# Kernel optimization log

Hardware: AMD Instinct MI355X
Metric: run time of the kernel (lower is better)

The kernel has to match this reference:

```python
import jax, jax.numpy as jnp
import numpy as np

N = 1_000_000   # active voxels
CIN = 32
COUT = 64
K = 9           # 3x3 kernel offsets (rulebook size)
EPS = 1e-5


def setup_inputs() -> dict:
    key = jax.random.key(0)
    ks = jax.random.split(key, 6)
    x = jax.random.normal(ks[0], (N, CIN), dtype=jnp.float32)
    # rulebook: neighbor index per (voxel, kernel offset); stride=1 so same coord set
    nbr = jax.random.randint(ks[1], (N, K), 0, N, dtype=jnp.int32)
    W1 = jax.random.normal(ks[2], (K, CIN, COUT), dtype=jnp.float32) * (1.0 / np.sqrt(K * CIN))
    W2 = jax.random.normal(ks[3], (K, COUT, COUT), dtype=jnp.float32) * (1.0 / np.sqrt(K * COUT))
    Wd = jax.random.normal(ks[4], (CIN, COUT), dtype=jnp.float32) * (1.0 / np.sqrt(CIN))
    g1 = jnp.ones((COUT,), jnp.float32); b1 = jnp.zeros((COUT,), jnp.float32)
    g2 = jnp.ones((COUT,), jnp.float32); b2 = jnp.zeros((COUT,), jnp.float32)
    gd = jnp.ones((COUT,), jnp.float32); bd = jnp.zeros((COUT,), jnp.float32)
    return {"x": x, "W1": W1, "g1": g1, "b1": b1, "W2": W2, "g2": g2, "b2": b2,
            "Wd": Wd, "gd": gd, "bd": bd, "nbr": nbr}


def _sparse_conv(x, nbr, W):
    # gather-GEMM-scatter; loop over the fixed K=9 kernel offsets to avoid
    # materializing the full [N, K, Cin] gathered tensor
    out = jnp.zeros((x.shape[0], W.shape[-1]), dtype=x.dtype)
    for k in range(W.shape[0]):
        out = out + jnp.take(x, nbr[:, k], axis=0) @ W[k]
    return out


def _bn(x, gamma, beta):
    # BatchNorm1d over the voxel dimension (training-mode batch statistics)
    mu = jnp.mean(x, axis=0)
    var = jnp.var(x, axis=0)
    return gamma * (x - mu) * jax.lax.rsqrt(var + EPS) + beta


def reference(x, W1, g1, b1, W2, g2, b2, Wd, gd, bd, nbr):
    # downsample branch (1x1 conv -> BN, no relu) since in_ch != out_ch
    identity = _bn(x @ Wd, gd, bd)
    # conv1: SparseConv3x3 -> BN -> ReLU
    out = jax.nn.relu(_bn(_sparse_conv(x, nbr, W1), g1, b1))
    # conv2: SparseConv3x3 -> BN (no relu)
    out = _bn(_sparse_conv(out, nbr, W2), g2, b2)
    # residual add + final ReLU
    return jax.nn.relu(out + identity)
```

## Files before the change

kernel.cpp:

```cpp
#include <hip/hip_runtime.h>
#include <hip/hip_bf16.h>

#define NV 1000000
#define CI 32
#define CO 64
#define KK 9
#define NG (NV / 16)
#define EPSV 1e-5f

typedef __bf16 bf16x8 __attribute__((ext_vector_type(8)));
typedef float  f32x4  __attribute__((ext_vector_type(4)));

__device__ __forceinline__ f32x4 mfma16(bf16x8 a, bf16x8 b, f32x4 c) {
    return __builtin_amdgcn_mfma_f32_16x16x32_bf16(a, b, c, 0, 0, 0);
}

__device__ __forceinline__ float xredseg(float v) {
    v += __shfl_xor(v, 16, 64);
    v += __shfl_xor(v, 32, 64);
    return v;
}

__global__ void k_prep_w(const float* __restrict__ W1, const float* __restrict__ W2,
                         const float* __restrict__ Wd,
                         __bf16* __restrict__ W1T, __bf16* __restrict__ W2T,
                         __bf16* __restrict__ WdT) {
    int i = blockIdx.x * blockDim.x + threadIdx.x;
    const int n1 = KK * CO * CI;
    const int n2 = KK * CO * CO;
    const int nd = CO * CI;
    if (i < n1) {
        int k = i / (CO * CI), r = i % (CO * CI), co = r / CI, ci = r % CI;
        W1T[i] = (__bf16)W1[(k * CI + ci) * CO + co];
    } else if (i < n1 + n2) {
        int j = i - n1;
        int k = j / (CO * CO), r = j % (CO * CO), co = r / CO, ci = r % CO;
        W2T[j] = (__bf16)W2[(k * CO + ci) * CO + co];
    } else if (i < n1 + n2 + nd) {
        int j = i - n1 - n2;
        int co = j / CI, ci = j % CI;
        WdT[j] = (__bf16)Wd[ci * CO + co];
    }
}

__global__ void k_prep_x(const float* __restrict__ x, __bf16* __restrict__ xb) {
    int i = blockIdx.x * blockDim.x + threadIdx.x;
    const float4* px = (const float4*)x + 2 * (size_t)i;
    float4 u = px[0], v = px[1];
    bf16x8 o;
    o[0] = (__bf16)u.x; o[1] = (__bf16)u.y; o[2] = (__bf16)u.z; o[3] = (__bf16)u.w;
    o[4] = (__bf16)v.x; o[5] = (__bf16)v.y; o[6] = (__bf16)v.z; o[7] = (__bf16)v.w;
    *((bf16x8*)xb + i) = o;
}

__global__ __launch_bounds__(256, 2) void k_conv1(
    const __bf16* __restrict__ xb, const int* __restrict__ nbr,
    const __bf16* __restrict__ W1T, const __bf16* __restrict__ WdT,
    __bf16* __restrict__ y1b, float* __restrict__ stats) {
    __shared__ __align__(16) char w1smem[KK * CO * CI * 2];

    const int lane = threadIdx.x & 63;
    const int w    = threadIdx.x >> 6;
    const int r    = lane & 15;
    const int seg  = lane >> 4;

#pragma unroll
    for (int j = 0; j < 9; j++) {
        const __bf16* srcp = W1T + (size_t)(j * 256 + threadIdx.x) * 8;
        __builtin_amdgcn_global_load_lds(
            (const __attribute__((address_space(1))) void*)srcp,
            (__attribute__((address_space(3))) void*)(w1smem + j * 4096 + w * 1024),
            16, 0, 0);
    }
    __syncthreads();

    bf16x8 wd[4];
#pragma unroll
    for (int t = 0; t < 4; t++)
        wd[t] = *(const bf16x8*)(WdT + (size_t)(t * 16 + r) * CI + seg * 8);

    float ps1[4] = {0.f,0.f,0.f,0.f}, pq1[4] = {0.f,0.f,0.f,0.f};
    float psd[4] = {0.f,0.f,0.f,0.f}, pqd[4] = {0.f,0.f,0.f,0.f};

    const int slot   = blockIdx.x * 4 + w;
    const int stride = gridDim.x * 4;
    const f32x4 z = {0.f, 0.f, 0.f, 0.f};

    auto loadIdx = [&](int (&idx)[KK], int tile) {
        const int* nb = nbr + (size_t)(tile * 16 + r) * KK;
#pragma unroll
        for (int k = 0; k < KK; k++) idx[k] = nb[k];
    };
    auto gather9 = [&](bf16x8 (&g)[KK], const int (&idx)[KK]) {
#pragma unroll
        for (int k = 0; k < KK; k++)
            g[k] = *(const bf16x8*)(xb + (size_t)idx[k] * CI + seg * 8);
    };
    auto loadAd = [&](int tile) {
        return *(const bf16x8*)(xb + (size_t)(tile * 16 + r) * CI + seg * 8);
    };
    auto compute = [&](int tile, const bf16x8 (&g)[KK], bf16x8 ad) {
        int w1off = 0;
        asm volatile("" : "+v"(w1off));
        const __bf16* wb = (const __bf16*)w1smem + w1off;

        f32x4 acc[4]  = {z, z, z, z};
        f32x4 accd[4] = {z, z, z, z};
#pragma unroll
        for (int t = 0; t < 4; t++) accd[t] = mfma16(ad, wd[t], accd[t]);
#pragma unroll
        for (int k = 0; k < KK; k++) {
#pragma unroll
            for (int t = 0; t < 4; t++) {
                bf16x8 b = *(const bf16x8*)(wb + k * 2048 + t * 512 + r * 32 + seg * 8);
                acc[t] = mfma16(g[k], b, acc[t]);
            }
        }

        const int vb = tile * 16;
#pragma unroll
        for (int t = 0; t < 4; t++) {
#pragma unroll
            for (int rr = 0; rr < 4; rr++) {
                float val = acc[t][rr];
                int row = vb + seg * 4 + rr;
                __builtin_nontemporal_store((__bf16)val, &y1b[(size_t)row * CO + t * 16 + r]);
                ps1[t] += val; pq1[t] += val * val;
                float dv = accd[t][rr];
                psd[t] += dv; pqd[t] += dv * dv;
            }
        }
    };

    int idx0[KK], idx1[KK];
    bf16x8 g0[KK], g1[KK];
    bf16x8 ad0, ad1;

    int it = slot;
    loadIdx(idx0, it);
    gather9(g0, idx0); ad0 = loadAd(it);
    int itn = it + stride;
    bool have = (itn < NG);
    if (have) loadIdx(idx1, itn);

    while (true) {
        if (have) {
            gather9(g1, idx1); ad1 = loadAd(itn);
            int it2 = itn + stride;
            if (it2 < NG) loadIdx(idx0, it2);
        }
        compute(it, g0, ad0);
        if (!have) break;
        it = itn; itn = it + stride; have = (itn < NG);

        if (have) {
            gather9(g0, idx0); ad0 = loadAd(itn);
            int it2 = itn + stride;
            if (it2 < NG) loadIdx(idx1, it2);
        }
        compute(it, g1, ad1);
        if (!have) break;
        it = itn; itn = it + stride; have = (itn < NG);
    }

#pragma unroll
    for (int t = 0; t < 4; t++) {
        ps1[t] = xredseg(ps1[t]); pq1[t] = xredseg(pq1[t]);
        psd[t] = xredseg(psd[t]); pqd[t] = xredseg(pqd[t]);
    }
    if (lane < 16) {
#pragma unroll
        for (int t = 0; t < 4; t++) {
            atomicAdd(&stats[0 * 64 + t * 16 + lane], ps1[t]);
            atomicAdd(&stats[1 * 64 + t * 16 + lane], pq1[t]);
            atomicAdd(&stats[2 * 64 + t * 16 + lane], psd[t]);
            atomicAdd(&stats[3 * 64 + t * 16 + lane], pqd[t]);
        }
    }
}

#define TILE_B (16 * KK * 128)

__global__ __launch_bounds__(128, 2) void k_conv2(
    const __bf16* __restrict__ h1b, const int* __restrict__ nbr,
    const __bf16* __restrict__ W2T, const float* __restrict__ g1,
    const float* __restrict__ b1,
    float* __restrict__ y2, float* __restrict__ stats) {
    __shared__ __align__(16) char smem[2][TILE_B];

    const int lane = threadIdx.x & 63;
    const int w    = threadIdx.x >> 6;
    const int r    = lane & 15;
    const int seg  = lane >> 4;
    const int p    = lane & 7;

    bf16x8 w2[KK][2][2];
#pragma unroll
    for (int k = 0; k < KK; k++)
#pragma unroll
        for (int t2 = 0; t2 < 2; t2++)
#pragma unroll
            for (int s = 0; s < 2; s++) {
                int co = w * 32 + t2 * 16 + r;
                int ci = s * 32 + seg * 8;
                w2[k][t2][s] = *(const bf16x8*)(W2T + ((size_t)(k * CO + co)) * CO + ci);
            }

    float scP[8], shP[8];
#pragma unroll
    for (int j = 0; j < 8; j++) {
        int c0 = p * 8 + j;
        float mu  = stats[c0] * (1.0f / NV);
        float var = stats[64 + c0] * (1.0f / NV) - mu * mu;
        float s   = g1[c0] * rsqrtf(var + EPSV);
        scP[j] = s; shP[j] = b1[c0] - mu * s;
    }

    int ri[9], dstoff[9];
#pragma unroll
    for (int s = 0; s < 9; s++) {
        int c = w * 576 + s * 64 + lane;
        int rIdx = c >> 3;
        int i = (rIdx * 57) >> 9;
        ri[s] = rIdx;
        dstoff[s] = rIdx * 128 + ((p ^ (i & 7)) * 16);
    }

    auto loadIdx = [&](int (&ix)[9], int tile) {
        const int* nb = nbr + (size_t)tile * (16 * KK);
#pragma unroll
        for (int s = 0; s < 9; s++) ix[s] = nb[ri[s]];
    };
    auto loadDat = [&](f32x4 (&d)[9], const int (&ix)[9]) {
#pragma unroll
        for (int s = 0; s < 9; s++)
            d[s] = *(const f32x4*)(h1b + (size_t)ix[s] * CO + p * 8);
    };
    auto xform = [&](char* tb, const f32x4 (&d)[9]) {
#pragma unroll
        for (int s = 0; s < 9; s++) {
            union { f32x4 f; bf16x8 b; } u; u.f = d[s];
            bf16x8 o;
#pragma unroll
            for (int j = 0; j < 8; j++)
                o[j] = (__bf16)fmaxf((float)u.b[j] * scP[j] + shP[j], 0.f);
            *(bf16x8*)(tb + dstoff[s]) = o;
        }
    };

    float ps[2] = {0.f, 0.f}, pq[2] = {0.f, 0.f};
    const f32x4 z = {0.f, 0.f, 0.f, 0.f};
    const int sw = r & 7;
    const int G = gridDim.x;

    int idxN[9]; f32x4 dat[9];
    int it = blockIdx.x;
    loadIdx(idxN, it);
    loadDat(dat, idxN);
    { int t1 = it + G;     loadIdx(idxN, t1 < NG ? t1 : NG - 1); }
    xform(smem[0], dat);
    loadDat(dat, idxN);
    { int t2 = it + 2 * G; loadIdx(idxN, t2 < NG ? t2 : NG - 1); }
    __syncthreads();
    int cur = 0;

    for (; it < NG; it += G) {
        const __bf16* base = (const __bf16*)smem[cur];
        f32x4 acc[2] = {z, z};
#pragma unroll
        for (int k = 0; k < KK; k++) {
            const __bf16* rp = base + (size_t)(r * KK + k) * 64;
            bf16x8 a0 = *(const bf16x8*)(rp + ((seg ^ sw) * 8));
            bf16x8 a1 = *(const bf16x8*)(rp + (((4 + seg) ^ sw) * 8));
            acc[0] = mfma16(a0, w2[k][0][0], acc[0]);
            acc[0] = mfma16(a1, w2[k][0][1], acc[0]);
            acc[1] = mfma16(a0, w2[k][1][0], acc[1]);
            acc[1] = mfma16(a1, w2[k][1][1], acc[1]);
        }

        const int vb = it * 16;
#pragma unroll
        for (int t2 = 0; t2 < 2; t2++) {
#pragma unroll
            for (int rr = 0; rr < 4; rr++) {
                float val = acc[t2][rr];
                int row = vb + seg * 4 + rr;
                int c = w * 32 + t2 * 16 + r;
                __builtin_nontemporal_store(val, &y2[(size_t)row * CO + c]);
                ps[t2] += val; pq[t2] += val * val;
            }
        }

        int nx = it + G;
        if (nx < NG) {
            xform(smem[cur ^ 1], dat);
            loadDat(dat, idxN);
            { int t3 = it + 3 * G; loadIdx(idxN, t3 < NG ? t3 : NG - 1); }
            __syncthreads();
            cur ^= 1;
        }
    }

#pragma unroll
    for (int t2 = 0; t2 < 2; t2++) { ps[t2] = xredseg(ps[t2]); pq[t2] = xredseg(pq[t2]); }
    if (lane < 16) {
#pragma unroll
        for (int t2 = 0; t2 < 2; t2++) {
            atomicAdd(&stats[4 * 64 + w * 32 + t2 * 16 + lane], ps[t2]);
            atomicAdd(&stats[5 * 64 + w * 32 + t2 * 16 + lane], pq[t2]);
        }
    }
}

__global__ __launch_bounds__(256, 2) void k_final(
    const __bf16* __restrict__ xb, const __bf16* __restrict__ WdT,
    float* __restrict__ out, const float* __restrict__ stats,
    const float* __restrict__ g2, const float* __restrict__ b2,
    const float* __restrict__ gd, const float* __restrict__ bd) {
    __shared__ float s2[CO], sh2[CO], sdv[CO], shd[CO];
    int t = threadIdx.x;
    if (t < CO) {
        float mu2  = stats[4 * 64 + t] * (1.0f / NV);
        float var2 = stats[5 * 64 + t] * (1.0f / NV) - mu2 * mu2;
        float s = g2[t] * rsqrtf(var2 + EPSV);
        s2[t] = s; sh2[t] = b2[t] - mu2 * s;
        float mud  = stats[2 * 64 + t] * (1.0f / NV);
        float vard = stats[3 * 64 + t] * (1.0f / NV) - mud * mud;
        float sd = gd[t] * rsqrtf(vard + EPSV);
        sdv[t] = sd; shd[t] = bd[t] - mud * sd;
    }
    __syncthreads();

    const int lane = threadIdx.x & 63;
    const int w    = threadIdx.x >> 6;
    const int r    = lane & 15;
    const int seg  = lane >> 4;

    bf16x8 wd[4];
#pragma unroll
    for (int t4 = 0; t4 < 4; t4++)
        wd[t4] = *(const bf16x8*)(WdT + (size_t)(t4 * 16 + r) * CI + seg * 8);

    const int slot = blockIdx.x * 4 + w;
    const int nslots = gridDim.x * 4;
    const f32x4 z = {0.f, 0.f, 0.f, 0.f};

    for (int gid = slot; gid < NG; gid += nslots) {
        const int vb = gid * 16;
        const int v  = vb + r;
        bf16x8 ad = *(const bf16x8*)(xb + (size_t)v * CI + seg * 8);
        f32x4 accd[4] = {z, z, z, z};
#pragma unroll
        for (int t4 = 0; t4 < 4; t4++) accd[t4] = mfma16(ad, wd[t4], accd[t4]);
#pragma unroll
        for (int t4 = 0; t4 < 4; t4++) {
#pragma unroll
            for (int rr = 0; rr < 4; rr++) {
                int row = vb + seg * 4 + rr;
                int c = t4 * 16 + r;
                size_t o = (size_t)row * CO + c;
                float y2v = out[o];
                float res = s2[c] * y2v + sh2[c] + sdv[c] * accd[t4][rr] + shd[c];
                out[o] = fmaxf(res, 0.f);
            }
        }
    }
}

extern "C" void kernel_launch(void* const* d_in, const int* in_sizes, int n_in,
                              void* d_out, int out_size, void* d_ws, size_t ws_size,
                              hipStream_t stream) {
    const float* x  = (const float*)d_in[0];
    const float* W1 = (const float*)d_in[1];
    const float* g1 = (const float*)d_in[2];
    const float* b1 = (const float*)d_in[3];
    const float* W2 = (const float*)d_in[4];
    const float* g2 = (const float*)d_in[5];
    const float* b2 = (const float*)d_in[6];
    const float* Wd = (const float*)d_in[7];
    const float* gd = (const float*)d_in[8];
    const float* bd = (const float*)d_in[9];
    const int*  nbr = (const int*)d_in[10];

    char* ws = (char*)d_ws;
    __bf16* xb  = (__bf16*)ws;
    __bf16* y1b = (__bf16*)(ws + 64000000);
    __bf16* W1T = (__bf16*)(ws + 192000000);
    __bf16* W2T = W1T + KK * CO * CI;
    __bf16* WdT = W2T + KK * CO * CO;
    float* stats = (float*)(ws + 192000000 + 2 * (KK*CO*CI + KK*CO*CO + CO*CI));

    hipMemsetAsync(stats, 0, 6 * 64 * sizeof(float), stream);

    int nprep = KK*CO*CI + KK*CO*CO + CO*CI;
    k_prep_w<<<(nprep + 255) / 256, 256, 0, stream>>>(W1, W2, Wd, W1T, W2T, WdT);
    k_prep_x<<<(NV * CI / 8) / 256, 256, 0, stream>>>(x, xb);
    k_conv1<<<1024, 256, 0, stream>>>(xb, nbr, W1T, WdT, y1b, stats);
    k_conv2<<<1024, 128, 0, stream>>>(y1b, nbr, W2T, g1, b1, (float*)d_out, stats);
    k_final<<<1024, 256, 0, stream>>>(xb, WdT, (float*)d_out, stats, g2, b2, gd, bd);
}
```

Baseline: 617.1 us.

## Swap MFMA operands for row-contiguous vector stores and store conv2 output as bf16

The MFMA operands are swapped so each lane holds four consecutive output channels of one voxel. Each lane can then write them with a single vector store instead of four scattered scalar stores in conv1, conv2 and the final kernel. conv2 now writes its intermediate as bf16 into a new workspace region when the workspace is large enough, which halves that round-trip traffic. The per-channel stats reduction is reworked for the new layout, and the conv1 grid shrinks to 768 blocks. The bf16 intermediate adds rounding error to the conv2 output before the final BN.

```diff
diff --git a/kernel.cpp b/kernel.cpp
--- a/kernel.cpp
+++ b/kernel.cpp
@@ -9,6 +9,7 @@
 #define EPSV 1e-5f
 
 typedef __bf16 bf16x8 __attribute__((ext_vector_type(8)));
+typedef __bf16 bf16x4 __attribute__((ext_vector_type(4)));
 typedef float  f32x4  __attribute__((ext_vector_type(4)));
 
 __device__ __forceinline__ f32x4 mfma16(bf16x8 a, bf16x8 b, f32x4 c) {
@@ -18,6 +19,13 @@
 __device__ __forceinline__ float xredseg(float v) {
     v += __shfl_xor(v, 16, 64);
     v += __shfl_xor(v, 32, 64);
+    return v;
+}
+__device__ __forceinline__ float xred16(float v) {
+    v += __shfl_xor(v, 1, 64);
+    v += __shfl_xor(v, 2, 64);
+    v += __shfl_xor(v, 4, 64);
+    v += __shfl_xor(v, 8, 64);
     return v;
 }
 
@@ -79,7 +87,11 @@
     for (int t = 0; t < 4; t++)
         wd[t] = *(const bf16x8*)(WdT + (size_t)(t * 16 + r) * CI + seg * 8);
 
-    float ps1[4] = {0.f,0.f,0.f,0.f}, pq1[4] = {0.f,0.f,0.f,0.f};
+    float ps1[4][4], pq1[4][4];
+#pragma unroll
+    for (int t = 0; t < 4; t++)
+#pragma unroll
+        for (int rr = 0; rr < 4; rr++) { ps1[t][rr] = 0.f; pq1[t][rr] = 0.f; }
     float psd[4] = {0.f,0.f,0.f,0.f}, pqd[4] = {0.f,0.f,0.f,0.f};
 
     const int slot   = blockIdx.x * 4 + w;
@@ -113,22 +125,23 @@
 #pragma unroll
             for (int t = 0; t < 4; t++) {
                 bf16x8 b = *(const bf16x8*)(wb + k * 2048 + t * 512 + r * 32 + seg * 8);
-                acc[t] = mfma16(g[k], b, acc[t]);
+                acc[t] = mfma16(b, g[k], acc[t]);
             }
         }
 
         const int vb = tile * 16;
 #pragma unroll
         for (int t = 0; t < 4; t++) {
+            bf16x4 o;
 #pragma unroll
             for (int rr = 0; rr < 4; rr++) {
                 float val = acc[t][rr];
-                int row = vb + seg * 4 + rr;
-                __builtin_nontemporal_store((__bf16)val, &y1b[(size_t)row * CO + t * 16 + r]);
-                ps1[t] += val; pq1[t] += val * val;
+                o[rr] = (__bf16)val;
+                ps1[t][rr] += val; pq1[t][rr] += val * val;
                 float dv = accd[t][rr];
                 psd[t] += dv; pqd[t] += dv * dv;
             }
+            *(bf16x4*)(y1b + (size_t)(vb + r) * CO + t * 16 + seg * 4) = o;
         }
     };
 
@@ -164,15 +177,27 @@
     }
 
 #pragma unroll
-    for (int t = 0; t < 4; t++) {
-        ps1[t] = xredseg(ps1[t]); pq1[t] = xredseg(pq1[t]);
-        psd[t] = xredseg(psd[t]); pqd[t] = xredseg(pqd[t]);
-    }
+    for (int t = 0; t < 4; t++)
+#pragma unroll
+        for (int rr = 0; rr < 4; rr++) {
+            ps1[t][rr] = xred16(ps1[t][rr]);
+            pq1[t][rr] = xred16(pq1[t][rr]);
+        }
+    if (r == 0) {
+#pragma unroll
+        for (int t = 0; t < 4; t++)
+#pragma unroll
+            for (int rr = 0; rr < 4; rr++) {
+                int ch = t * 16 + seg * 4 + rr;
+                atomicAdd(&stats[0 * 64 + ch], ps1[t][rr]);
+                atomicAdd(&stats[1 * 64 + ch], pq1[t][rr]);
+            }
+    }
+#pragma unroll
+    for (int t = 0; t < 4; t++) { psd[t] = xredseg(psd[t]); pqd[t] = xredseg(pqd[t]); }
     if (lane < 16) {
 #pragma unroll
         for (int t = 0; t < 4; t++) {
-            atomicAdd(&stats[0 * 64 + t * 16 + lane], ps1[t]);
-            atomicAdd(&stats[1 * 64 + t * 16 + lane], pq1[t]);
             atomicAdd(&stats[2 * 64 + t * 16 + lane], psd[t]);
             atomicAdd(&stats[3 * 64 + t * 16 + lane], pqd[t]);
         }
@@ -181,11 +206,13 @@
 
 #define TILE_B (16 * KK * 128)
 
+template <bool BF16OUT>
 __global__ __launch_bounds__(128, 2) void k_conv2(
     const __bf16* __restrict__ h1b, const int* __restrict__ nbr,
     const __bf16* __restrict__ W2T, const float* __restrict__ g1,
     const float* __restrict__ b1,
-    float* __restrict__ y2, float* __restrict__ stats) {
+    __bf16* __restrict__ y2b, float* __restrict__ y2f,
+    float* __restrict__ stats) {
     __shared__ __align__(16) char smem[2][TILE_B];
 
     const int lane = threadIdx.x & 63;
@@ -248,7 +275,11 @@
         }
     };
 
-    float ps[2] = {0.f, 0.f}, pq[2] = {0.f, 0.f};
+    float ps[2][4], pq[2][4];
+#pragma unroll
+    for (int t2 = 0; t2 < 2; t2++)
+#pragma unroll
+        for (int rr = 0; rr < 4; rr++) { ps[t2][rr] = 0.f; pq[t2][rr] = 0.f; }
     const f32x4 z = {0.f, 0.f, 0.f, 0.f};
     const int sw = r & 7;
     const int G = gridDim.x;
@@ -272,22 +303,32 @@
             const __bf16* rp = base + (size_t)(r * KK + k) * 64;
             bf16x8 a0 = *(const bf16x8*)(rp + ((seg ^ sw) * 8));
             bf16x8 a1 = *(const bf16x8*)(rp + (((4 + seg) ^ sw) * 8));
-            acc[0] = mfma16(a0, w2[k][0][0], acc[0]);
-            acc[0] = mfma16(a1, w2[k][0][1], acc[0]);
-            acc[1] = mfma16(a0, w2[k][1][0], acc[1]);
-            acc[1] = mfma16(a1, w2[k][1][1], acc[1]);
+            acc[0] = mfma16(w2[k][0][0], a0, acc[0]);
+            acc[0] = mfma16(w2[k][0][1], a1, acc[0]);
+            acc[1] = mfma16(w2[k][1][0], a0, acc[1]);
+            acc[1] = mfma16(w2[k][1][1], a1, acc[1]);
         }
 
         const int vb = it * 16;
 #pragma unroll
         for (int t2 = 0; t2 < 2; t2++) {
-#pragma unroll
-            for (int rr = 0; rr < 4; rr++) {
-                float val = acc[t2][rr];
-                int row = vb + seg * 4 + rr;
-                int c = w * 32 + t2 * 16 + r;
-                __builtin_nontemporal_store(val, &y2[(size_t)row * CO + c]);
-                ps[t2] += val; pq[t2] += val * val;
+            size_t off = (size_t)(vb + r) * CO + w * 32 + t2 * 16 + seg * 4;
+            if constexpr (BF16OUT) {
+                bf16x4 o;
+#pragma unroll
+                for (int rr = 0; rr < 4; rr++) {
+                    float val = acc[t2][rr];
+                    o[rr] = (__bf16)val;
+                    ps[t2][rr] += val; pq[t2][rr] += val * val;
+                }
+                *(bf16x4*)(y2b + off) = o;
+            } else {
+#pragma unroll
+                for (int rr = 0; rr < 4; rr++) {
+                    float val = acc[t2][rr];
+                    ps[t2][rr] += val; pq[t2][rr] += val * val;
+                }
+                *(f32x4*)(y2f + off) = acc[t2];
             }
         }
 
@@ -302,32 +343,42 @@
     }
 
 #pragma unroll
-    for (int t2 = 0; t2 < 2; t2++) { ps[t2] = xredseg(ps[t2]); pq[t2] = xredseg(pq[t2]); }
-    if (lane < 16) {
-#pragma unroll
-        for (int t2 = 0; t2 < 2; t2++) {
-            atomicAdd(&stats[4 * 64 + w * 32 + t2 * 16 + lane], ps[t2]);
-            atomicAdd(&stats[5 * 64 + w * 32 + t2 * 16 + lane], pq[t2]);
-        }
-    }
-}
-
+    for (int t2 = 0; t2 < 2; t2++)
+#pragma unroll
+        for (int rr = 0; rr < 4; rr++) {
+            ps[t2][rr] = xred16(ps[t2][rr]);
+            pq[t2][rr] = xred16(pq[t2][rr]);
+        }
+    if (r == 0) {
+#pragma unroll
+        for (int t2 = 0; t2 < 2; t2++)
+#pragma unroll
+            for (int rr = 0; rr < 4; rr++) {
+                int ch = w * 32 + t2 * 16 + seg * 4 + rr;
+                atomicAdd(&stats[4 * 64 + ch], ps[t2][rr]);
+                atomicAdd(&stats[5 * 64 + ch], pq[t2][rr]);
+            }
+    }
+}
+
+template <bool BF16IN>
 __global__ __launch_bounds__(256, 2) void k_final(
     const __bf16* __restrict__ xb, const __bf16* __restrict__ WdT,
+    const __bf16* __restrict__ y2b,
     float* __restrict__ out, const float* __restrict__ stats,
     const float* __restrict__ g2, const float* __restrict__ b2,
     const float* __restrict__ gd, const float* __restrict__ bd) {
-    __shared__ float s2[CO], sh2[CO], sdv[CO], shd[CO];
+    __shared__ float s2[CO], shc[CO], sdv[CO];
     int t = threadIdx.x;
     if (t < CO) {
         float mu2  = stats[4 * 64 + t] * (1.0f / NV);
         float var2 = stats[5 * 64 + t] * (1.0f / NV) - mu2 * mu2;
         float s = g2[t] * rsqrtf(var2 + EPSV);
-        s2[t] = s; sh2[t] = b2[t] - mu2 * s;
         float mud  = stats[2 * 64 + t] * (1.0f / NV);
         float vard = stats[3 * 64 + t] * (1.0f / NV) - mud * mud;
         float sd = gd[t] * rsqrtf(vard + EPSV);
-        sdv[t] = sd; shd[t] = bd[t] - mud * sd;
+        s2[t] = s; sdv[t] = sd;
+        shc[t] = (b2[t] - mu2 * s) + (bd[t] - mud * sd);
     }
     __syncthreads();
 
@@ -347,22 +398,31 @@
 
     for (int gid = slot; gid < NG; gid += nslots) {
         const int vb = gid * 16;
-        const int v  = vb + r;
-        bf16x8 ad = *(const bf16x8*)(xb + (size_t)v * CI + seg * 8);
+        bf16x8 ad = *(const bf16x8*)(xb + (size_t)(vb + r) * CI + seg * 8);
         f32x4 accd[4] = {z, z, z, z};
 #pragma unroll
-        for (int t4 = 0; t4 < 4; t4++) accd[t4] = mfma16(ad, wd[t4], accd[t4]);
+        for (int t4 = 0; t4 < 4; t4++) accd[t4] = mfma16(wd[t4], ad, accd[t4]);
+
 #pragma unroll
         for (int t4 = 0; t4 < 4; t4++) {
-#pragma unroll
-            for (int rr = 0; rr < 4; rr++) {
-                int row = vb + seg * 4 + rr;
-                int c = t4 * 16 + r;
-                size_t o = (size_t)row * CO + c;
-                float y2v = out[o];
-                float res = s2[c] * y2v + sh2[c] + sdv[c] * accd[t4][rr] + shd[c];
-                out[o] = fmaxf(res, 0.f);
-            }
+            int cb = t4 * 16 + seg * 4;
+            size_t off = (size_t)(vb + r) * CO + cb;
+            f32x4 yv;
+            if constexpr (BF16IN) {
+                bf16x4 yb = *(const bf16x4*)(y2b + off);
+#pragma unroll
+                for (int rr = 0; rr < 4; rr++) yv[rr] = (float)yb[rr];
+            } else {
+                yv = *(const f32x4*)(out + off);
+            }
+            f32x4 s2v  = *(const f32x4*)&s2[cb];
+            f32x4 shcv = *(const f32x4*)&shc[cb];
+            f32x4 sdvv = *(const f32x4*)&sdv[cb];
+            f32x4 o;
+#pragma unroll
+            for (int rr = 0; rr < 4; rr++)
+                o[rr] = fmaxf(s2v[rr] * yv[rr] + shcv[rr] + sdvv[rr] * accd[t4][rr], 0.f);
+            *(f32x4*)(out + off) = o;
         }
     }
 }
@@ -389,13 +449,25 @@
     __bf16* W2T = W1T + KK * CO * CI;
     __bf16* WdT = W2T + KK * CO * CO;
     float* stats = (float*)(ws + 192000000 + 2 * (KK*CO*CI + KK*CO*CO + CO*CI));
+    size_t y2off = ((192000000 + 2 * (KK*CO*CI + KK*CO*CO + CO*CI) + 6*64*4) + 255) & ~(size_t)255;
+    __bf16* y2b = (__bf16*)(ws + y2off);
+    bool bf16y2 = (ws_size >= y2off + (size_t)NV * CO * 2 + 256);
 
     hipMemsetAsync(stats, 0, 6 * 64 * sizeof(float), stream);
 
     int nprep = KK*CO*CI + KK*CO*CO + CO*CI;
     k_prep_w<<<(nprep + 255) / 256, 256, 0, stream>>>(W1, W2, Wd, W1T, W2T, WdT);
     k_prep_x<<<(NV * CI / 8) / 256, 256, 0, stream>>>(x, xb);
-    k_conv1<<<1024, 256, 0, stream>>>(xb, nbr, W1T, WdT, y1b, stats);
-    k_conv2<<<1024, 128, 0, stream>>>(y1b, nbr, W2T, g1, b1, (float*)d_out, stats);
-    k_final<<<1024, 256, 0, stream>>>(xb, WdT, (float*)d_out, stats, g2, b2, gd, bd);
-}
+    k_conv1<<<768, 256, 0, stream>>>(xb, nbr, W1T, WdT, y1b, stats);
+    if (bf16y2) {
+        k_conv2<true><<<1024, 128, 0, stream>>>(y1b, nbr, W2T, g1, b1,
+                                                y2b, nullptr, stats);
+        k_final<true><<<1024, 256, 0, stream>>>(xb, WdT, y2b, (float*)d_out, stats,
+                                                g2, b2, gd, bd);
+    } else {
+        k_conv2<false><<<1024, 128, 0, stream>>>(y1b, nbr, W2T, g1, b1,
+                                                 nullptr, (float*)d_out, stats);
+        k_final<false><<<1024, 256, 0, stream>>>(xb, WdT, nullptr, (float*)d_out, stats,
+                                                 g2, b2, gd, bd);
+    }
+}
```

Result: slower. 957.2 us (+55.1%).
